# Kernel optimization log

Hardware: AMD Instinct MI355X
Metric: run time of the kernel (lower is better)

The kernel has to match this reference:

```python
import jax, jax.numpy as jnp
import numpy as np

B, N, D, H = 4096, 64, 32, 64

def setup_inputs() -> dict:
    key = jax.random.key(0)
    ks = jax.random.split(key, 10)
    s = lambda fan_in: 1.0 / np.sqrt(fan_in)
    return {
        "joint_features": jax.random.normal(ks[0], (B, N, D), jnp.float32),
        "Wm1": jax.random.uniform(ks[1], (2 * D, H), jnp.float32, -s(2 * D), s(2 * D)),
        "bm1": jax.random.uniform(ks[2], (H,), jnp.float32, -s(2 * D), s(2 * D)),
        "Wm2": jax.random.uniform(ks[3], (H, D), jnp.float32, -s(H), s(H)),
        "bm2": jax.random.uniform(ks[4], (D,), jnp.float32, -s(H), s(H)),
        "Wu1": jax.random.uniform(ks[5], (2 * D, H), jnp.float32, -s(2 * D), s(2 * D)),
        "bu1": jax.random.uniform(ks[6], (H,), jnp.float32, -s(2 * D), s(2 * D)),
        "Wu2": jax.random.uniform(ks[7], (H, D), jnp.float32, -s(H), s(H)),
        "bu2": jax.random.uniform(ks[8], (D,), jnp.float32, -s(H), s(H)),
        "residual_weight": jnp.float32(0.5),
        "num_joints": N,
    }

def reference(joint_features, Wm1, bm1, Wm2, bm2, Wu1, bu1, Wu2, bu2, residual_weight, num_joints):
    n = num_joints
    # chain topology: directed edges (i->i+1) and (i+1->i); dst receives message
    dst = jnp.concatenate([jnp.arange(n - 1), jnp.arange(1, n)])  # [E]
    src = jnp.concatenate([jnp.arange(1, n), jnp.arange(n - 1)])  # [E]
    # edge gather + concat: [B, E, 2D]
    edge_in = jnp.concatenate([joint_features[:, dst], joint_features[:, src]], axis=-1)
    # message MLP (ReLU after both layers, per original Sequential)
    msg = jax.nn.relu(jax.nn.relu(edge_in @ Wm1 + bm1) @ Wm2 + bm2)  # [B, E, D]
    # scatter-add messages to destination nodes
    messages = jnp.zeros_like(joint_features).at[:, dst].add(msg)  # [B, N, D]
    # per-node update MLP on concat(feature, message)
    upd_in = jnp.concatenate([joint_features, messages], axis=-1)  # [B, N, 2D]
    updated = jax.nn.relu(upd_in @ Wu1 + bu1) @ Wu2 + bu2  # [B, N, D]
    return residual_weight * updated + (1.0 - residual_weight) * joint_features
```

## Files before the change

kernel.cpp:

```cpp
#include <hip/hip_runtime.h>
#include <hip/hip_bf16.h>


typedef __bf16 bf16x8 __attribute__((ext_vector_type(8)));
typedef float  f32x4  __attribute__((ext_vector_type(4)));
typedef unsigned short u16;

#define NBATCH 8
#define NBI 2
#define ITERS (NBATCH / NBI)
#define HS  72
#define MBS 40
#define XS  36

__device__ __forceinline__ u16 f2b(float f) { return __builtin_bit_cast(u16, (__bf16)f); }
__device__ __forceinline__ f32x4 MFMA(bf16x8 a, bf16x8 b, f32x4 c) {
    return __builtin_amdgcn_mfma_f32_16x16x32_bf16(a, b, c, 0, 0, 0);
}
__device__ __forceinline__ bf16x8 pack8(float4 a, float4 b) {
    bf16x8 r = {(__bf16)a.x, (__bf16)a.y, (__bf16)a.z, (__bf16)a.w,
                (__bf16)b.x, (__bf16)b.y, (__bf16)b.z, (__bf16)b.w};
    return r;
}
__device__ __forceinline__ uint2 relu_pack4(f32x4 acc, f32x4 bias) {
    uint2 o;
    o.x = (unsigned)f2b(fmaxf(acc[0] + bias[0], 0.f)) |
          ((unsigned)f2b(fmaxf(acc[1] + bias[1], 0.f)) << 16);
    o.y = (unsigned)f2b(fmaxf(acc[2] + bias[2], 0.f)) |
          ((unsigned)f2b(fmaxf(acc[3] + bias[3], 0.f)) << 16);
    return o;
}
__device__ __forceinline__ void wave_lds_fence() {
    asm volatile("s_waitcnt lgkmcnt(0)" ::: "memory");
}
__device__ __forceinline__ void barrier_lds() {
    asm volatile("s_waitcnt lgkmcnt(0)" ::: "memory");
    __builtin_amdgcn_s_barrier();
    asm volatile("" ::: "memory");
}

__global__ __launch_bounds__(256, 2)
void agn_mfma(const float* __restrict__ x, const float* __restrict__ Wm1,
              const float* __restrict__ bm1, const float* __restrict__ Wm2,
              const float* __restrict__ bm2, const float* __restrict__ Wu1,
              const float* __restrict__ bu1, const float* __restrict__ Wu2,
              const float* __restrict__ bu2, const float* __restrict__ rw_p,
              float* __restrict__ out)
{
    __shared__ __align__(16) u16   sH[256 * HS];
    __shared__ __align__(16) u16   sMB[256 * MBS];
    __shared__ __align__(16) float sX[128 * XS];

    const int t = threadIdx.x;
    const int w = t >> 6;
    const int lane = t & 63;
    const int ln = lane & 15;
    const int q  = lane >> 4;

    bf16x8 B1a[4], B1b[4], B2[2][2], B3[2][4], B4[2][2];
#pragma unroll
    for (int nt = 0; nt < 4; ++nt)
#pragma unroll
        for (int j = 0; j < 8; ++j) {
            B1a[nt][j] = (__bf16)Wm1[(q * 8 + j) * 64 + nt * 16 + ln];
            B1b[nt][j] = (__bf16)Wm1[(32 + q * 8 + j) * 64 + nt * 16 + ln];
        }
#pragma unroll
    for (int s = 0; s < 2; ++s)
#pragma unroll
        for (int nt = 0; nt < 2; ++nt)
#pragma unroll
            for (int j = 0; j < 8; ++j)
                B2[s][nt][j] = (__bf16)Wm2[(s * 32 + q * 8 + j) * 32 + nt * 16 + ln];
#pragma unroll
    for (int s = 0; s < 2; ++s)
#pragma unroll
        for (int nt = 0; nt < 4; ++nt)
#pragma unroll
            for (int j = 0; j < 8; ++j)
                B3[s][nt][j] = (__bf16)Wu1[(s * 32 + q * 8 + j) * 64 + nt * 16 + ln];
#pragma unroll
    for (int s = 0; s < 2; ++s)
#pragma unroll
        for (int nt = 0; nt < 2; ++nt)
#pragma unroll
            for (int j = 0; j < 8; ++j)
                B4[s][nt][j] = (__bf16)Wu2[(s * 32 + q * 8 + j) * 32 + nt * 16 + ln];

    f32x4 bm1s[4], bu1s[4], bm2s[2], bu2s[2];
#pragma unroll
    for (int ht = 0; ht < 4; ++ht)
#pragma unroll
        for (int r = 0; r < 4; ++r) {
            bm1s[ht][r] = bm1[ht * 16 + q * 4 + r];
            bu1s[ht][r] = bu1[ht * 16 + q * 4 + r];
        }
#pragma unroll
    for (int s = 0; s < 2; ++s)
#pragma unroll
        for (int r = 0; r < 4; ++r) {
            bm2s[s][r] = bm2[s * 16 + q * 4 + r];
            bu2s[s][r] = bu2[s * 16 + q * 4 + r];
        }
    const float rw = rw_p[0];
    const float om = 1.f - rw;

    const size_t base = (size_t)blockIdx.x * (NBATCH * 64 * 32);

    for (int it = 0; it < ITERS; ++it) {
        const float* xit = x + base + (size_t)it * (NBI * 64 * 32);
        float*       oit = out + base + (size_t)it * (NBI * 64 * 32);

        {
            const int row = t >> 1;
            const int cb  = (t & 1) * 16;
            const float* src = xit + row * 32 + cb;
            float* dstp = &sX[row * XS + cb];
            float4 v0 = *(const float4*)(src);
            float4 v1 = *(const float4*)(src + 4);
            float4 v2 = *(const float4*)(src + 8);
            float4 v3 = *(const float4*)(src + 12);
            *(float4*)(dstp)      = v0;
            *(float4*)(dstp + 4)  = v1;
            *(float4*)(dstp + 8)  = v2;
            *(float4*)(dstp + 12) = v3;
        }
        barrier_lds();

#pragma unroll
        for (int m = 0; m < 4; ++m) {
            const int erow = (4 * w + m) * 16 + ln;
            const int bb = erow >> 7;
            int e = erow & 127;
            if (e >= 126) e = 0;
            const int dst  = (e < 63) ? e : e - 62;
            const int srcn = (e < 63) ? e + 1 : e - 63;
            const float* pd = &sX[((bb << 6) + dst) * XS + q * 8];
            const float* ps = &sX[((bb << 6) + srcn) * XS + q * 8];
            float4 d0 = *(const float4*)pd;
            float4 d1 = *(const float4*)(pd + 4);
            float4 s0 = *(const float4*)ps;
            float4 s1 = *(const float4*)(ps + 4);
            bf16x8 Ad = pack8(d0, d1);
            bf16x8 As = pack8(s0, s1);
            u16* rowp = &sH[erow * HS];
#pragma unroll
            for (int ht = 0; ht < 4; ++ht) {
                f32x4 acc = {0.f, 0.f, 0.f, 0.f};
                acc = MFMA(B1a[ht], Ad, acc);
                acc = MFMA(B1b[ht], As, acc);
                *(uint2*)&rowp[ht * 16 + q * 4] = relu_pack4(acc, bm1s[ht]);
            }
        }
        wave_lds_fence();

#pragma unroll
        for (int m = 0; m < 4; ++m) {
            const int row = (4 * w + m) * 16 + ln;
            bf16x8 A0 = __builtin_bit_cast(bf16x8, *(const uint4*)&sH[row * HS + q * 8]);
            bf16x8 A1 = __builtin_bit_cast(bf16x8, *(const uint4*)&sH[row * HS + 32 + q * 8]);
#pragma unroll
            for (int s = 0; s < 2; ++s) {
                f32x4 acc = {0.f, 0.f, 0.f, 0.f};
                acc = MFMA(B2[0][s], A0, acc);
                acc = MFMA(B2[1][s], A1, acc);
                *(uint2*)&sMB[row * MBS + s * 16 + q * 4] = relu_pack4(acc, bm2s[s]);
            }
        }
        barrier_lds();

#pragma unroll
        for (int m = 0; m < 2; ++m) {
            const int row = (2 * w + m) * 16 + ln;
            const int bb = row >> 6;
            const int i2 = row & 63;
            const float* p = &sX[row * XS + q * 8];
            float4 a0 = *(const float4*)p;
            float4 a1 = *(const float4*)(p + 4);
            bf16x8 A0 = pack8(a0, a1);
            float mv[8] = {0.f, 0.f, 0.f, 0.f, 0.f, 0.f, 0.f, 0.f};
            if (i2 < 63) {
                uint4 u = *(const uint4*)&sMB[((bb << 7) + i2) * MBS + q * 8];
                const unsigned* pu = (const unsigned*)&u;
#pragma unroll
                for (int h = 0; h < 4; ++h) {
                    mv[2 * h]     += __uint_as_float(pu[h] << 16);
                    mv[2 * h + 1] += __uint_as_float(pu[h] & 0xFFFF0000u);
                }
            }
            if (i2 > 0) {
                uint4 u = *(const uint4*)&sMB[((bb << 7) + 62 + i2) * MBS + q * 8];
                const unsigned* pu = (const unsigned*)&u;
#pragma unroll
                for (int h = 0; h < 4; ++h) {
                    mv[2 * h]     += __uint_as_float(pu[h] << 16);
                    mv[2 * h + 1] += __uint_as_float(pu[h] & 0xFFFF0000u);
                }
            }
            bf16x8 A1;
#pragma unroll
            for (int j = 0; j < 8; ++j) A1[j] = (__bf16)mv[j];
#pragma unroll
            for (int ht = 0; ht < 4; ++ht) {
                f32x4 acc = {0.f, 0.f, 0.f, 0.f};
                acc = MFMA(B3[0][ht], A0, acc);
                acc = MFMA(B3[1][ht], A1, acc);
                *(uint2*)&sH[row * HS + ht * 16 + q * 4] = relu_pack4(acc, bu1s[ht]);
            }
        }
        wave_lds_fence();

#pragma unroll
        for (int m = 0; m < 2; ++m) {
            const int row = (2 * w + m) * 16 + ln;
            bf16x8 A0 = __builtin_bit_cast(bf16x8, *(const uint4*)&sH[row * HS + q * 8]);
            bf16x8 A1 = __builtin_bit_cast(bf16x8, *(const uint4*)&sH[row * HS + 32 + q * 8]);
#pragma unroll
            for (int s = 0; s < 2; ++s) {
                f32x4 acc = {0.f, 0.f, 0.f, 0.f};
                acc = MFMA(B4[0][s], A0, acc);
                acc = MFMA(B4[1][s], A1, acc);
                f32x4 xv = *(const f32x4*)&sX[row * XS + s * 16 + q * 4];
                float4 o;
                o.x = rw * (acc[0] + bu2s[s][0]) + om * xv[0];
                o.y = rw * (acc[1] + bu2s[s][1]) + om * xv[1];
                o.z = rw * (acc[2] + bu2s[s][2]) + om * xv[2];
                o.w = rw * (acc[3] + bu2s[s][3]) + om * xv[3];
                *(float4*)(oit + row * 32 + s * 16 + q * 4) = o;
            }
        }
        barrier_lds();
    }
}

extern "C" void kernel_launch(void* const* d_in, const int* in_sizes, int n_in,
                              void* d_out, int out_size, void* d_ws, size_t ws_size,
                              hipStream_t stream) {
    const float* x   = (const float*)d_in[0];
    const float* Wm1 = (const float*)d_in[1];
    const float* bm1 = (const float*)d_in[2];
    const float* Wm2 = (const float*)d_in[3];
    const float* bm2 = (const float*)d_in[4];
    const float* Wu1 = (const float*)d_in[5];
    const float* bu1 = (const float*)d_in[6];
    const float* Wu2 = (const float*)d_in[7];
    const float* bu2 = (const float*)d_in[8];
    const float* rw  = (const float*)d_in[9];
    float* out = (float*)d_out;

    const int B = in_sizes[0] / (64 * 32);
    agn_mfma<<<B / NBATCH, 256, 0, stream>>>(x, Wm1, bm1, Wm2, bm2, Wu1, bu1, Wu2, bu2, rw, out);
}
```

Baseline: 117.7 us.

## Process one batch per iteration with register prefetch and higher occupancy

Each block now handles one batch element per iteration instead of two, and 4 batches per block instead of 8, so LDS buffers shrink by half. The launch bound rises to 3 blocks per CU. The next batch's input is prefetched into registers while the current batch computes, hiding the global load latency. The trade-off is less MFMA work per barrier, more blocks that each reload the weights into registers, and tighter register limits under the higher occupancy target.

```diff
diff --git a/kernel.cpp b/kernel.cpp
--- a/kernel.cpp
+++ b/kernel.cpp
@@ -6,9 +6,8 @@
 typedef float  f32x4  __attribute__((ext_vector_type(4)));
 typedef unsigned short u16;
 
-#define NBATCH 8
-#define NBI 2
-#define ITERS (NBATCH / NBI)
+#define NBATCH 4
+#define ITERS  NBATCH
 #define HS  72
 #define MBS 40
 #define XS  36
@@ -39,7 +38,7 @@
     asm volatile("" ::: "memory");
 }
 
-__global__ __launch_bounds__(256, 2)
+__global__ __launch_bounds__(256, 3)
 void agn_mfma(const float* __restrict__ x, const float* __restrict__ Wm1,
               const float* __restrict__ bm1, const float* __restrict__ Wm2,
               const float* __restrict__ bm2, const float* __restrict__ Wu1,
@@ -47,9 +46,9 @@
               const float* __restrict__ bu2, const float* __restrict__ rw_p,
               float* __restrict__ out)
 {
-    __shared__ __align__(16) u16   sH[256 * HS];
-    __shared__ __align__(16) u16   sMB[256 * MBS];
-    __shared__ __align__(16) float sX[128 * XS];
+    __shared__ __align__(16) u16   sH[128 * HS];
+    __shared__ __align__(16) u16   sMB[128 * MBS];
+    __shared__ __align__(16) float sX[64 * XS];
 
     const int t = threadIdx.x;
     const int w = t >> 6;
@@ -107,36 +106,39 @@
 
     const size_t base = (size_t)blockIdx.x * (NBATCH * 64 * 32);
 
+    float4 p0, p1;
+    {
+        const float* xp = x + base + t * 8;
+        p0 = *(const float4*)xp;
+        p1 = *(const float4*)(xp + 4);
+    }
+
     for (int it = 0; it < ITERS; ++it) {
-        const float* xit = x + base + (size_t)it * (NBI * 64 * 32);
-        float*       oit = out + base + (size_t)it * (NBI * 64 * 32);
+        const float* xit = x + base + (size_t)it * (64 * 32);
+        float*       oit = out + base + (size_t)it * (64 * 32);
 
         {
-            const int row = t >> 1;
-            const int cb  = (t & 1) * 16;
-            const float* src = xit + row * 32 + cb;
-            float* dstp = &sX[row * XS + cb];
-            float4 v0 = *(const float4*)(src);
-            float4 v1 = *(const float4*)(src + 4);
-            float4 v2 = *(const float4*)(src + 8);
-            float4 v3 = *(const float4*)(src + 12);
-            *(float4*)(dstp)      = v0;
-            *(float4*)(dstp + 4)  = v1;
-            *(float4*)(dstp + 8)  = v2;
-            *(float4*)(dstp + 12) = v3;
+            float* dstp = &sX[(t >> 2) * XS + (t & 3) * 8];
+            *(float4*)dstp       = p0;
+            *(float4*)(dstp + 4) = p1;
         }
         barrier_lds();
 
-#pragma unroll
-        for (int m = 0; m < 4; ++m) {
-            const int erow = (4 * w + m) * 16 + ln;
-            const int bb = erow >> 7;
-            int e = erow & 127;
+        if (it + 1 < ITERS) {
+            const float* xn = xit + 64 * 32 + t * 8;
+            p0 = *(const float4*)xn;
+            p1 = *(const float4*)(xn + 4);
+        }
+
+#pragma unroll
+        for (int m = 0; m < 2; ++m) {
+            const int erow = (2 * w + m) * 16 + ln;
+            int e = erow;
             if (e >= 126) e = 0;
             const int dst  = (e < 63) ? e : e - 62;
             const int srcn = (e < 63) ? e + 1 : e - 63;
-            const float* pd = &sX[((bb << 6) + dst) * XS + q * 8];
-            const float* ps = &sX[((bb << 6) + srcn) * XS + q * 8];
+            const float* pd = &sX[dst * XS + q * 8];
+            const float* ps = &sX[srcn * XS + q * 8];
             float4 d0 = *(const float4*)pd;
             float4 d1 = *(const float4*)(pd + 4);
             float4 s0 = *(const float4*)ps;
@@ -155,8 +157,8 @@
         wave_lds_fence();
 
 #pragma unroll
-        for (int m = 0; m < 4; ++m) {
-            const int row = (4 * w + m) * 16 + ln;
+        for (int m = 0; m < 2; ++m) {
+            const int row = (2 * w + m) * 16 + ln;
             bf16x8 A0 = __builtin_bit_cast(bf16x8, *(const uint4*)&sH[row * HS + q * 8]);
             bf16x8 A1 = __builtin_bit_cast(bf16x8, *(const uint4*)&sH[row * HS + 32 + q * 8]);
 #pragma unroll
@@ -169,18 +171,15 @@
         }
         barrier_lds();
 
-#pragma unroll
-        for (int m = 0; m < 2; ++m) {
-            const int row = (2 * w + m) * 16 + ln;
-            const int bb = row >> 6;
-            const int i2 = row & 63;
+        {
+            const int row = w * 16 + ln;
             const float* p = &sX[row * XS + q * 8];
             float4 a0 = *(const float4*)p;
             float4 a1 = *(const float4*)(p + 4);
             bf16x8 A0 = pack8(a0, a1);
             float mv[8] = {0.f, 0.f, 0.f, 0.f, 0.f, 0.f, 0.f, 0.f};
-            if (i2 < 63) {
-                uint4 u = *(const uint4*)&sMB[((bb << 7) + i2) * MBS + q * 8];
+            if (row < 63) {
+                uint4 u = *(const uint4*)&sMB[row * MBS + q * 8];
                 const unsigned* pu = (const unsigned*)&u;
 #pragma unroll
                 for (int h = 0; h < 4; ++h) {
@@ -188,8 +187,8 @@
                     mv[2 * h + 1] += __uint_as_float(pu[h] & 0xFFFF0000u);
                 }
             }
-            if (i2 > 0) {
-                uint4 u = *(const uint4*)&sMB[((bb << 7) + 62 + i2) * MBS + q * 8];
+            if (row > 0) {
+                uint4 u = *(const uint4*)&sMB[(62 + row) * MBS + q * 8];
                 const unsigned* pu = (const unsigned*)&u;
 #pragma unroll
                 for (int h = 0; h < 4; ++h) {
@@ -210,9 +209,8 @@
         }
         wave_lds_fence();
 
-#pragma unroll
-        for (int m = 0; m < 2; ++m) {
-            const int row = (2 * w + m) * 16 + ln;
+        {
+            const int row = w * 16 + ln;
             bf16x8 A0 = __builtin_bit_cast(bf16x8, *(const uint4*)&sH[row * HS + q * 8]);
             bf16x8 A1 = __builtin_bit_cast(bf16x8, *(const uint4*)&sH[row * HS + 32 + q * 8]);
 #pragma unroll
```

Result: slower. 144.7 us (+22.9%).
